# Performance work log

Hardware: AMD Instinct MI355X
Metric: run time of the kernel (lower is better)

The kernel has to match this reference:

```python
import jax, jax.numpy as jnp
import numpy as np

D_MODEL = 1024
NUM_HEADS = 16
DEPTH = D_MODEL // NUM_HEADS


def setup_inputs() -> dict:
    key = jax.random.key(0)
    ks = jax.random.split(key, 9)
    B, S = 2, 2048
    s = 1.0 / np.sqrt(D_MODEL)
    return {
        "x": jax.random.normal(ks[0], (B, S, D_MODEL), dtype=jnp.float32),
        "wq": jax.random.normal(ks[1], (D_MODEL, D_MODEL), dtype=jnp.float32) * s,
        "bq": jnp.zeros((D_MODEL,), dtype=jnp.float32),
        "wk": jax.random.normal(ks[2], (D_MODEL, D_MODEL), dtype=jnp.float32) * s,
        "bk": jnp.zeros((D_MODEL,), dtype=jnp.float32),
        "wv": jax.random.normal(ks[3], (D_MODEL, D_MODEL), dtype=jnp.float32) * s,
        "bv": jnp.zeros((D_MODEL,), dtype=jnp.float32),
        "wo": jax.random.normal(ks[4], (D_MODEL, D_MODEL), dtype=jnp.float32) * s,
        "bo": jnp.zeros((D_MODEL,), dtype=jnp.float32),
    }


def _split_heads(t):
    # [B, S, D] -> [B, H, S, depth]
    B, S, _ = t.shape
    return t.reshape(B, S, NUM_HEADS, DEPTH).transpose(0, 2, 1, 3)


def reference(x, wq, bq, wk, bk, wv, bv, wo, bo):
    B, S, _ = x.shape
    q = _split_heads(x @ wq + bq)
    k = _split_heads(x @ wk + bk)
    v = _split_heads(x @ wv + bv)
    scale = 1.0 / jnp.sqrt(jnp.asarray(DEPTH, dtype=x.dtype))
    logits = jnp.einsum("bhsd,bhtd->bhst", q, k) * scale  # [B,H,S,S]
    attn = jax.nn.softmax(logits, axis=-1)
    ctx = jnp.einsum("bhst,bhtd->bhsd", attn, v)  # [B,H,S,depth]
    concat = ctx.transpose(0, 2, 1, 3).reshape(B, S, D_MODEL)
    return concat @ wo + bo
```

## Files before the change

### kernel.cpp

```cpp
#include <hip/hip_runtime.h>
#include <hip/hip_bf16.h>

typedef __bf16 bf16;
typedef __bf16 bf16x4 __attribute__((ext_vector_type(4)));
typedef __bf16 bf16x8 __attribute__((ext_vector_type(8)));
typedef float f32x4 __attribute__((ext_vector_type(4)));

#define D_MODEL 1024
#define NHEAD 16
#define DEPTH 64
#define SEQ 2048
#define BATCH 2
#define NTOK (BATCH * SEQ)

#define Q_SCALE 0.18033688f

__global__ __launch_bounds__(256) void convert_f32_bf16(const float* __restrict__ src,
                                                        bf16* __restrict__ dst) {
    int i = blockIdx.x * 256 + threadIdx.x;
    float4 v = ((const float4*)src)[i];
    bf16x4 o = {(bf16)v.x, (bf16)v.y, (bf16)v.z, (bf16)v.w};
    *(bf16x4*)&dst[(size_t)i * 4] = o;
}

__global__ __launch_bounds__(256) void transpose_convert(const float* __restrict__ w0,
                                                         const float* __restrict__ w1,
                                                         const float* __restrict__ w2,
                                                         const float* __restrict__ w3,
                                                         bf16* __restrict__ dst) {
    int z = blockIdx.z;
    const float* w = (z == 0) ? w0 : (z == 1) ? w1 : (z == 2) ? w2 : w3;
    bf16* d = dst + (size_t)z * D_MODEL * D_MODEL;
    __shared__ float tile[32][33];
    int c0 = blockIdx.x * 32;
    int r0 = blockIdx.y * 32;
    int tx = threadIdx.x, ty = threadIdx.y;
#pragma unroll
    for (int i = 0; i < 4; i++)
        tile[ty + i * 8][tx] = w[(size_t)(r0 + ty + i * 8) * D_MODEL + c0 + tx];
    __syncthreads();
#pragma unroll
    for (int i = 0; i < 4; i++)
        d[(size_t)(c0 + ty + i * 8) * D_MODEL + r0 + tx] = (bf16)tile[tx][ty + i * 8];
}

__device__ __forceinline__ void gemm_core(const bf16* __restrict__ A,
                                          const bf16* __restrict__ Bt,
                                          int row0, int col0,
                                          bf16* As, bf16* Bs, f32x4 acc[4][4]) {
    const int tid = threadIdx.x;
    const int lane = tid & 63, wave = tid >> 6;
    const int quad = lane >> 4, l16 = lane & 15;
    const int wm = (wave & 1) << 6, wn = (wave >> 1) << 6;
    const int sr = tid >> 1, sh = (tid & 1) << 4;

    for (int k0 = 0; k0 < D_MODEL; k0 += 32) {
        bf16x8 a0 = *(const bf16x8*)&A[(size_t)(row0 + sr) * D_MODEL + k0 + sh];
        bf16x8 a1 = *(const bf16x8*)&A[(size_t)(row0 + sr) * D_MODEL + k0 + sh + 8];
        bf16x8 b0 = *(const bf16x8*)&Bt[(size_t)(col0 + sr) * D_MODEL + k0 + sh];
        bf16x8 b1 = *(const bf16x8*)&Bt[(size_t)(col0 + sr) * D_MODEL + k0 + sh + 8];
        __syncthreads();
        *(bf16x8*)&As[sr * 40 + sh] = a0;
        *(bf16x8*)&As[sr * 40 + sh + 8] = a1;
        *(bf16x8*)&Bs[sr * 40 + sh] = b0;
        *(bf16x8*)&Bs[sr * 40 + sh + 8] = b1;
        __syncthreads();
        bf16x8 af[4], bfr[4];
#pragma unroll
        for (int i = 0; i < 4; i++)
            af[i] = *(const bf16x8*)&As[(wm + i * 16 + l16) * 40 + quad * 8];
#pragma unroll
        for (int j = 0; j < 4; j++)
            bfr[j] = *(const bf16x8*)&Bs[(wn + j * 16 + l16) * 40 + quad * 8];
#pragma unroll
        for (int i = 0; i < 4; i++)
#pragma unroll
            for (int j = 0; j < 4; j++)
                acc[i][j] = __builtin_amdgcn_mfma_f32_16x16x32_bf16(af[i], bfr[j], acc[i][j], 0, 0, 0);
    }
}

__global__ __launch_bounds__(256) void qkv_gemm(const bf16* __restrict__ xb,
                                                const bf16* __restrict__ wtb,
                                                const float* __restrict__ bq,
                                                const float* __restrict__ bk,
                                                const float* __restrict__ bv,
                                                bf16* __restrict__ q,
                                                bf16* __restrict__ k,
                                                bf16* __restrict__ v) {
    __shared__ bf16 As[128 * 40];
    __shared__ bf16 Bs[128 * 40];
    int z = blockIdx.z;
    const bf16* Bt = wtb + (size_t)z * D_MODEL * D_MODEL;
    const float* bias = (z == 0) ? bq : (z == 1) ? bk : bv;
    int row0 = blockIdx.y * 128, col0 = blockIdx.x * 128;
    f32x4 acc[4][4] = {};
    gemm_core(xb, Bt, row0, col0, As, Bs, acc);

    const int lane = threadIdx.x & 63, wave = threadIdx.x >> 6;
    const int quad = lane >> 4, l16 = lane & 15;
    const int wm = (wave & 1) << 6, wn = (wave >> 1) << 6;
    bf16* dst = (z == 0) ? q : (z == 1) ? k : v;
    const float sc = (z == 0) ? Q_SCALE : 1.0f;
#pragma unroll
    for (int i = 0; i < 4; i++) {
#pragma unroll
        for (int j = 0; j < 4; j++) {
            int colg = col0 + wn + j * 16 + l16;
            int hh = colg >> 6, d = colg & 63;
            float bi = bias[colg];
            int rbase = row0 + wm + i * 16 + quad * 4;
            int b = rbase >> 11;
            int sb = rbase & 2047;
            if (z < 2) {
#pragma unroll
                for (int r = 0; r < 4; r++) {
                    size_t idx = ((size_t)(b * NHEAD + hh) * SEQ + sb + r) * DEPTH + d;
                    dst[idx] = (bf16)((acc[i][j][r] + bi) * sc);
                }
            } else {
                bf16x4 pv = {(bf16)(acc[i][j][0] + bi), (bf16)(acc[i][j][1] + bi),
                             (bf16)(acc[i][j][2] + bi), (bf16)(acc[i][j][3] + bi)};
                *(bf16x4*)&dst[((size_t)(b * NHEAD + hh) * DEPTH + d) * SEQ + sb] = pv;
            }
        }
    }
}

__global__ __launch_bounds__(256) void attn(const bf16* __restrict__ q,
                                            const bf16* __restrict__ k,
                                            const bf16* __restrict__ v,
                                            bf16* __restrict__ ctx) {
    __shared__ bf16 Ks[64 * 72];
    __shared__ bf16 Vs[64 * 72];
    __shared__ bf16 Ps[4][32 * 72];
    const int tid = threadIdx.x;
    const int lane = tid & 63, wave = tid >> 6;
    const int quad = lane >> 4, l16 = lane & 15;
    const int bh = blockIdx.y;
    const int q0 = blockIdx.x * 128;
    const size_t hb = (size_t)bh * SEQ * DEPTH;
    const bf16* qh = q + hb;
    const bf16* kh = k + hb;
    const bf16* vh = v + hb;

    bf16x8 bq_[2][2];
#pragma unroll
    for (int g = 0; g < 2; g++) {
        int qrow = q0 + wave * 32 + g * 16 + l16;
#pragma unroll
        for (int c = 0; c < 2; c++)
            bq_[g][c] = *(const bf16x8*)&qh[(size_t)qrow * DEPTH + c * 32 + quad * 8];
    }
    bf16* myP = &Ps[wave][0];

    bf16x8 ones;
#pragma unroll
    for (int i = 0; i < 8; i++) ones[i] = (bf16)1.0f;

    f32x4 ov[2][4] = {};
    f32x4 lacc[2] = {};

    const int srow = tid >> 2, scol = (tid & 3) << 4;
    const bf16* kg = kh + (size_t)srow * DEPTH + scol;
    const bf16* vg = vh + (size_t)srow * SEQ + scol;
    bf16* ksd = &Ks[srow * 72 + scol];
    bf16* vsd = &Vs[srow * 72 + scol];

    bf16x8 kr0 = *(const bf16x8*)kg, kr1 = *(const bf16x8*)(kg + 8);
    bf16x8 vr0 = *(const bf16x8*)vg, vr1 = *(const bf16x8*)(vg + 8);

    for (int t0 = 0; t0 < SEQ; t0 += 64) {
        __syncthreads();
        *(bf16x8*)ksd = kr0;  *(bf16x8*)(ksd + 8) = kr1;
        *(bf16x8*)vsd = vr0;  *(bf16x8*)(vsd + 8) = vr1;
        __syncthreads();
        if (t0 + 64 < SEQ) {
            const bf16* kgn = kg + (size_t)(t0 + 64) * DEPTH;
            const bf16* vgn = vg + (t0 + 64);
            kr0 = *(const bf16x8*)kgn;  kr1 = *(const bf16x8*)(kgn + 8);
            vr0 = *(const bf16x8*)vgn;  vr1 = *(const bf16x8*)(vgn + 8);
        }
        f32x4 sc[2][4] = {};
#pragma unroll
        for (int c = 0; c < 2; c++)
#pragma unroll
            for (int j = 0; j < 4; j++) {
                bf16x8 kf = *(const bf16x8*)&Ks[(j * 16 + l16) * 72 + c * 32 + quad * 8];
#pragma unroll
                for (int g = 0; g < 2; g++)
                    sc[g][j] = __builtin_amdgcn_mfma_f32_16x16x32_bf16(kf, bq_[g][c], sc[g][j], 0, 0, 0);
            }
#pragma unroll
        for (int g = 0; g < 2; g++)
#pragma unroll
            for (int j = 0; j < 4; j++) {
                bf16x4 pb = {(bf16)__builtin_amdgcn_exp2f(sc[g][j][0]),
                             (bf16)__builtin_amdgcn_exp2f(sc[g][j][1]),
                             (bf16)__builtin_amdgcn_exp2f(sc[g][j][2]),
                             (bf16)__builtin_amdgcn_exp2f(sc[g][j][3])};
                *(bf16x4*)&myP[(g * 16 + l16) * 72 + j * 16 + quad * 4] = pb;
            }
#pragma unroll
        for (int c = 0; c < 2; c++) {
            bf16x8 pf[2];
#pragma unroll
            for (int g = 0; g < 2; g++) {
                pf[g] = *(const bf16x8*)&myP[(g * 16 + l16) * 72 + c * 32 + quad * 8];
                lacc[g] = __builtin_amdgcn_mfma_f32_16x16x32_bf16(ones, pf[g], lacc[g], 0, 0, 0);
            }
#pragma unroll
            for (int t = 0; t < 4; t++) {
                bf16x8 vf = *(const bf16x8*)&Vs[(t * 16 + l16) * 72 + c * 32 + quad * 8];
#pragma unroll
                for (int g = 0; g < 2; g++)
                    ov[g][t] = __builtin_amdgcn_mfma_f32_16x16x32_bf16(vf, pf[g], ov[g][t], 0, 0, 0);
            }
        }
    }
    int b = bh >> 4, hh = bh & 15;
#pragma unroll
    for (int g = 0; g < 2; g++) {
        float inv = 1.0f / lacc[g][0];
        size_t rowb = ((size_t)(b * SEQ + q0 + wave * 32 + g * 16 + l16)) * D_MODEL + hh * 64;
#pragma unroll
        for (int t = 0; t < 4; t++) {
            bf16x4 ob = {(bf16)(ov[g][t][0] * inv), (bf16)(ov[g][t][1] * inv),
                         (bf16)(ov[g][t][2] * inv), (bf16)(ov[g][t][3] * inv)};
            *(bf16x4*)&ctx[rowb + t * 16 + quad * 4] = ob;
        }
    }
}

__global__ __launch_bounds__(256) void out_gemm(const bf16* __restrict__ ctx,
                                                const bf16* __restrict__ wot,
                                                const float* __restrict__ bo,
                                                float* __restrict__ out) {
    __shared__ bf16 As[128 * 40];
    __shared__ bf16 Bs[128 * 40];
    int row0 = blockIdx.y * 128, col0 = blockIdx.x * 128;
    f32x4 acc[4][4] = {};
    gemm_core(ctx, wot, row0, col0, As, Bs, acc);

    const int lane = threadIdx.x & 63, wave = threadIdx.x >> 6;
    const int quad = lane >> 4, l16 = lane & 15;
    const int wm = (wave & 1) << 6, wn = (wave >> 1) << 6;
#pragma unroll
    for (int i = 0; i < 4; i++)
#pragma unroll
        for (int j = 0; j < 4; j++) {
            int colg = col0 + wn + j * 16 + l16;
            float bi = bo[colg];
            int rbase = row0 + wm + i * 16 + quad * 4;
#pragma unroll
            for (int r = 0; r < 4; r++)
                out[(size_t)(rbase + r) * D_MODEL + colg] = acc[i][j][r] + bi;
        }
}

extern "C" void kernel_launch(void* const* d_in, const int* in_sizes, int n_in,
                              void* d_out, int out_size, void* d_ws, size_t ws_size,
                              hipStream_t stream) {
    const float* x  = (const float*)d_in[0];
    const float* wq = (const float*)d_in[1];
    const float* bq = (const float*)d_in[2];
    const float* wk = (const float*)d_in[3];
    const float* bk = (const float*)d_in[4];
    const float* wv = (const float*)d_in[5];
    const float* bv = (const float*)d_in[6];
    const float* wo = (const float*)d_in[7];
    const float* bo = (const float*)d_in[8];
    float* out = (float*)d_out;

    const size_t MB = 1024 * 1024;
    char* ws = (char*)d_ws;
    bf16* xb  = (bf16*)(ws);
    bf16* wtb = (bf16*)(ws + 8 * MB);
    bf16* qb  = (bf16*)(ws + 16 * MB);
    bf16* kb  = (bf16*)(ws + 24 * MB);
    bf16* vb  = (bf16*)(ws + 32 * MB);
    bf16* ctx = (bf16*)(ws + 40 * MB);

    convert_f32_bf16<<<NTOK * D_MODEL / 1024, 256, 0, stream>>>(x, xb);
    transpose_convert<<<dim3(32, 32, 4), dim3(32, 8), 0, stream>>>(wq, wk, wv, wo, wtb);
    qkv_gemm<<<dim3(8, 32, 3), 256, 0, stream>>>(xb, wtb, bq, bk, bv, qb, kb, vb);
    attn<<<dim3(SEQ / 128, BATCH * NHEAD), 256, 0, stream>>>(qb, kb, vb, ctx);
    out_gemm<<<dim3(8, 32), 256, 0, stream>>>(ctx, wtb + 3 * (size_t)D_MODEL * D_MODEL, bo, out);
}
```

Measured before the change: 208.8 us.

## Split attention over KV chunks with reduction kernel and use direct global-to-LDS GEMM loads

Attention is split into two KV chunks along a new grid dimension. Each chunk writes unnormalized fp32 partial outputs and row sums, and a new reduce kernel combines them into ctx. This is enabled only when the workspace is large enough. The GEMM core now loads tiles with global_load_lds straight into unpadded LDS, and the V projection uses swapped MFMA operands with a new scatter epilogue. The split raises occupancy but adds partial-buffer traffic and an extra launch, and the unpadded LDS may cause bank conflicts.

```diff
diff --git a/kernel.cpp b/kernel.cpp
--- a/kernel.cpp
+++ b/kernel.cpp
@@ -5,6 +5,9 @@
 typedef __bf16 bf16x4 __attribute__((ext_vector_type(4)));
 typedef __bf16 bf16x8 __attribute__((ext_vector_type(8)));
 typedef float f32x4 __attribute__((ext_vector_type(4)));
+
+typedef __attribute__((address_space(3))) void lds_void;
+typedef const __attribute__((address_space(1))) void gbl_void;
 
 #define D_MODEL 1024
 #define NHEAD 16
@@ -12,6 +15,7 @@
 #define SEQ 2048
 #define BATCH 2
 #define NTOK (BATCH * SEQ)
+#define ROWS (BATCH * NHEAD * SEQ)
 
 #define Q_SCALE 0.18033688f
 
@@ -44,6 +48,7 @@
         d[(size_t)(c0 + ty + i * 8) * D_MODEL + r0 + tx] = (bf16)tile[tx][ty + i * 8];
 }
 
+template <bool SWAP>
 __device__ __forceinline__ void gemm_core(const bf16* __restrict__ A,
                                           const bf16* __restrict__ Bt,
                                           int row0, int col0,
@@ -52,31 +57,33 @@
     const int lane = tid & 63, wave = tid >> 6;
     const int quad = lane >> 4, l16 = lane & 15;
     const int wm = (wave & 1) << 6, wn = (wave >> 1) << 6;
-    const int sr = tid >> 1, sh = (tid & 1) << 4;
+    const int srow = lane >> 2, selem = (lane & 3) * 8;
 
     for (int k0 = 0; k0 < D_MODEL; k0 += 32) {
-        bf16x8 a0 = *(const bf16x8*)&A[(size_t)(row0 + sr) * D_MODEL + k0 + sh];
-        bf16x8 a1 = *(const bf16x8*)&A[(size_t)(row0 + sr) * D_MODEL + k0 + sh + 8];
-        bf16x8 b0 = *(const bf16x8*)&Bt[(size_t)(col0 + sr) * D_MODEL + k0 + sh];
-        bf16x8 b1 = *(const bf16x8*)&Bt[(size_t)(col0 + sr) * D_MODEL + k0 + sh + 8];
         __syncthreads();
-        *(bf16x8*)&As[sr * 40 + sh] = a0;
-        *(bf16x8*)&As[sr * 40 + sh + 8] = a1;
-        *(bf16x8*)&Bs[sr * 40 + sh] = b0;
-        *(bf16x8*)&Bs[sr * 40 + sh + 8] = b1;
+#pragma unroll
+        for (int t = 0; t < 2; t++) {
+            int m = wave * 2 + t;
+            const bf16* ga = A + (size_t)(row0 + m * 16 + srow) * D_MODEL + k0 + selem;
+            const bf16* gb = Bt + (size_t)(col0 + m * 16 + srow) * D_MODEL + k0 + selem;
+            __builtin_amdgcn_global_load_lds((gbl_void*)ga, (lds_void*)(As + m * 512 + lane * 8), 16, 0, 0);
+            __builtin_amdgcn_global_load_lds((gbl_void*)gb, (lds_void*)(Bs + m * 512 + lane * 8), 16, 0, 0);
+        }
         __syncthreads();
         bf16x8 af[4], bfr[4];
 #pragma unroll
         for (int i = 0; i < 4; i++)
-            af[i] = *(const bf16x8*)&As[(wm + i * 16 + l16) * 40 + quad * 8];
+            af[i] = *(const bf16x8*)&As[(wm + i * 16 + l16) * 32 + quad * 8];
 #pragma unroll
         for (int j = 0; j < 4; j++)
-            bfr[j] = *(const bf16x8*)&Bs[(wn + j * 16 + l16) * 40 + quad * 8];
+            bfr[j] = *(const bf16x8*)&Bs[(wn + j * 16 + l16) * 32 + quad * 8];
 #pragma unroll
         for (int i = 0; i < 4; i++)
 #pragma unroll
             for (int j = 0; j < 4; j++)
-                acc[i][j] = __builtin_amdgcn_mfma_f32_16x16x32_bf16(af[i], bfr[j], acc[i][j], 0, 0, 0);
+                acc[i][j] = SWAP
+                    ? __builtin_amdgcn_mfma_f32_16x16x32_bf16(bfr[j], af[i], acc[i][j], 0, 0, 0)
+                    : __builtin_amdgcn_mfma_f32_16x16x32_bf16(af[i], bfr[j], acc[i][j], 0, 0, 0);
     }
 }
 
@@ -88,40 +95,53 @@
                                                 bf16* __restrict__ q,
                                                 bf16* __restrict__ k,
                                                 bf16* __restrict__ v) {
-    __shared__ bf16 As[128 * 40];
-    __shared__ bf16 Bs[128 * 40];
+    __shared__ bf16 As[128 * 32];
+    __shared__ bf16 Bs[128 * 32];
     int z = blockIdx.z;
     const bf16* Bt = wtb + (size_t)z * D_MODEL * D_MODEL;
     const float* bias = (z == 0) ? bq : (z == 1) ? bk : bv;
     int row0 = blockIdx.y * 128, col0 = blockIdx.x * 128;
     f32x4 acc[4][4] = {};
-    gemm_core(xb, Bt, row0, col0, As, Bs, acc);
 
     const int lane = threadIdx.x & 63, wave = threadIdx.x >> 6;
     const int quad = lane >> 4, l16 = lane & 15;
     const int wm = (wave & 1) << 6, wn = (wave >> 1) << 6;
-    bf16* dst = (z == 0) ? q : (z == 1) ? k : v;
-    const float sc = (z == 0) ? Q_SCALE : 1.0f;
-#pragma unroll
-    for (int i = 0; i < 4; i++) {
-#pragma unroll
-        for (int j = 0; j < 4; j++) {
-            int colg = col0 + wn + j * 16 + l16;
-            int hh = colg >> 6, d = colg & 63;
-            float bi = bias[colg];
-            int rbase = row0 + wm + i * 16 + quad * 4;
-            int b = rbase >> 11;
-            int sb = rbase & 2047;
-            if (z < 2) {
+
+    if (z < 2) {
+        gemm_core<false>(xb, Bt, row0, col0, As, Bs, acc);
+        bf16* dst = (z == 0) ? q : k;
+        const float sc = (z == 0) ? Q_SCALE : 1.0f;
+#pragma unroll
+        for (int i = 0; i < 4; i++) {
+#pragma unroll
+            for (int j = 0; j < 4; j++) {
+                int colg = col0 + wn + j * 16 + l16;
+                int hh = colg >> 6, d = colg & 63;
+                float bi = bias[colg];
+                int rbase = row0 + wm + i * 16 + quad * 4;
+                int b = rbase >> 11, sb = rbase & 2047;
 #pragma unroll
                 for (int r = 0; r < 4; r++) {
                     size_t idx = ((size_t)(b * NHEAD + hh) * SEQ + sb + r) * DEPTH + d;
                     dst[idx] = (bf16)((acc[i][j][r] + bi) * sc);
                 }
-            } else {
-                bf16x4 pv = {(bf16)(acc[i][j][0] + bi), (bf16)(acc[i][j][1] + bi),
-                             (bf16)(acc[i][j][2] + bi), (bf16)(acc[i][j][3] + bi)};
-                *(bf16x4*)&dst[((size_t)(b * NHEAD + hh) * DEPTH + d) * SEQ + sb] = pv;
+            }
+        }
+    } else {
+        gemm_core<true>(xb, Bt, row0, col0, As, Bs, acc);
+#pragma unroll
+        for (int i = 0; i < 4; i++) {
+            int tok = row0 + wm + i * 16 + l16;
+            int b = tok >> 11, sb = tok & 2047;
+#pragma unroll
+            for (int j = 0; j < 4; j++) {
+#pragma unroll
+                for (int r = 0; r < 4; r++) {
+                    int f = col0 + wn + j * 16 + quad * 4 + r;
+                    int hh = f >> 6, d = f & 63;
+                    v[((size_t)(b * NHEAD + hh) * DEPTH + d) * SEQ + sb] =
+                        (bf16)(acc[i][j][r] + bias[f]);
+                }
             }
         }
     }
@@ -130,7 +150,10 @@
 __global__ __launch_bounds__(256) void attn(const bf16* __restrict__ q,
                                             const bf16* __restrict__ k,
                                             const bf16* __restrict__ v,
-                                            bf16* __restrict__ ctx) {
+                                            bf16* __restrict__ ctx,
+                                            float* __restrict__ ovp,
+                                            float* __restrict__ lp,
+                                            int kv_chunk) {
     __shared__ bf16 Ks[64 * 72];
     __shared__ bf16 Vs[64 * 72];
     __shared__ bf16 Ps[4][32 * 72];
@@ -139,6 +162,8 @@
     const int quad = lane >> 4, l16 = lane & 15;
     const int bh = blockIdx.y;
     const int q0 = blockIdx.x * 128;
+    const int kv0 = blockIdx.z * kv_chunk;
+    const int kv_end = kv0 + kv_chunk;
     const size_t hb = (size_t)bh * SEQ * DEPTH;
     const bf16* qh = q + hb;
     const bf16* kh = k + hb;
@@ -167,15 +192,17 @@
     bf16* ksd = &Ks[srow * 72 + scol];
     bf16* vsd = &Vs[srow * 72 + scol];
 
-    bf16x8 kr0 = *(const bf16x8*)kg, kr1 = *(const bf16x8*)(kg + 8);
-    bf16x8 vr0 = *(const bf16x8*)vg, vr1 = *(const bf16x8*)(vg + 8);
-
-    for (int t0 = 0; t0 < SEQ; t0 += 64) {
+    bf16x8 kr0 = *(const bf16x8*)(kg + (size_t)kv0 * DEPTH);
+    bf16x8 kr1 = *(const bf16x8*)(kg + (size_t)kv0 * DEPTH + 8);
+    bf16x8 vr0 = *(const bf16x8*)(vg + kv0);
+    bf16x8 vr1 = *(const bf16x8*)(vg + kv0 + 8);
+
+    for (int t0 = kv0; t0 < kv_end; t0 += 64) {
         __syncthreads();
         *(bf16x8*)ksd = kr0;  *(bf16x8*)(ksd + 8) = kr1;
         *(bf16x8*)vsd = vr0;  *(bf16x8*)(vsd + 8) = vr1;
         __syncthreads();
-        if (t0 + 64 < SEQ) {
+        if (t0 + 64 < kv_end) {
             const bf16* kgn = kg + (size_t)(t0 + 64) * DEPTH;
             const bf16* vgn = vg + (t0 + 64);
             kr0 = *(const bf16x8*)kgn;  kr1 = *(const bf16x8*)(kgn + 8);
@@ -218,29 +245,64 @@
             }
         }
     }
+    if (ovp) {
+        size_t zb = (size_t)blockIdx.z * ROWS;
+#pragma unroll
+        for (int g = 0; g < 2; g++) {
+            int s = q0 + wave * 32 + g * 16 + l16;
+            size_t row = zb + (size_t)bh * SEQ + s;
+#pragma unroll
+            for (int t = 0; t < 4; t++)
+                *(f32x4*)&ovp[row * DEPTH + t * 16 + quad * 4] = ov[g][t];
+            if (quad == 0) lp[row] = lacc[g][0];
+        }
+    } else {
+        int b = bh >> 4, hh = bh & 15;
+#pragma unroll
+        for (int g = 0; g < 2; g++) {
+            float inv = 1.0f / lacc[g][0];
+            size_t rowb = ((size_t)(b * SEQ + q0 + wave * 32 + g * 16 + l16)) * D_MODEL + hh * 64;
+#pragma unroll
+            for (int t = 0; t < 4; t++) {
+                bf16x4 ob = {(bf16)(ov[g][t][0] * inv), (bf16)(ov[g][t][1] * inv),
+                             (bf16)(ov[g][t][2] * inv), (bf16)(ov[g][t][3] * inv)};
+                *(bf16x4*)&ctx[rowb + t * 16 + quad * 4] = ob;
+            }
+        }
+    }
+}
+
+__global__ __launch_bounds__(256) void reduce_ctx(const float* __restrict__ ovp,
+                                                  const float* __restrict__ lp,
+                                                  bf16* __restrict__ ctx,
+                                                  int ksplit) {
+    int idx = blockIdx.x * 256 + threadIdx.x;
+    int d4 = idx & 15;
+    size_t row = (size_t)(idx >> 4);
+    f32x4 o = {};
+    float l = 0.f;
+    for (int z = 0; z < ksplit; z++) {
+        o += *(const f32x4*)&ovp[((size_t)z * ROWS + row) * DEPTH + d4 * 4];
+        l += lp[(size_t)z * ROWS + row];
+    }
+    float inv = 1.0f / l;
+    int bh = (int)(row >> 11);
+    int s = (int)(row & 2047);
     int b = bh >> 4, hh = bh & 15;
-#pragma unroll
-    for (int g = 0; g < 2; g++) {
-        float inv = 1.0f / lacc[g][0];
-        size_t rowb = ((size_t)(b * SEQ + q0 + wave * 32 + g * 16 + l16)) * D_MODEL + hh * 64;
-#pragma unroll
-        for (int t = 0; t < 4; t++) {
-            bf16x4 ob = {(bf16)(ov[g][t][0] * inv), (bf16)(ov[g][t][1] * inv),
-                         (bf16)(ov[g][t][2] * inv), (bf16)(ov[g][t][3] * inv)};
-            *(bf16x4*)&ctx[rowb + t * 16 + quad * 4] = ob;
-        }
-    }
+    bf16x4 ob = {(bf16)(o[0] * inv), (bf16)(o[1] * inv),
+                 (bf16)(o[2] * inv), (bf16)(o[3] * inv)};
+    *(bf16x4*)&ctx[((size_t)(b * SEQ + s)) * D_MODEL + hh * 64 + d4 * 4] = ob;
 }
 
 __global__ __launch_bounds__(256) void out_gemm(const bf16* __restrict__ ctx,
                                                 const bf16* __restrict__ wot,
                                                 const float* __restrict__ bo,
                                                 float* __restrict__ out) {
-    __shared__ bf16 As[128 * 40];
-    __shared__ bf16 Bs[128 * 40];
+    __shared__ bf16 As[128 * 32];
+    __shared__ bf16 Bs[128 * 32];
     int row0 = blockIdx.y * 128, col0 = blockIdx.x * 128;
     f32x4 acc[4][4] = {};
-    gemm_core(ctx, wot, row0, col0, As, Bs, acc);
+    gemm_core<false>(ctx, wot, row0, col0, As, Bs, acc);
 
     const int lane = threadIdx.x & 63, wave = threadIdx.x >> 6;
     const int quad = lane >> 4, l16 = lane & 15;
@@ -280,10 +342,21 @@
     bf16* kb  = (bf16*)(ws + 24 * MB);
     bf16* vb  = (bf16*)(ws + 32 * MB);
     bf16* ctx = (bf16*)(ws + 40 * MB);
+    float* ovp = (float*)(ws + 48 * MB);
+    float* lp  = (float*)(ws + 82 * MB);
+
+    const int ksplit = (ws_size >= 84 * MB) ? 2 : 0;
 
     convert_f32_bf16<<<NTOK * D_MODEL / 1024, 256, 0, stream>>>(x, xb);
     transpose_convert<<<dim3(32, 32, 4), dim3(32, 8), 0, stream>>>(wq, wk, wv, wo, wtb);
     qkv_gemm<<<dim3(8, 32, 3), 256, 0, stream>>>(xb, wtb, bq, bk, bv, qb, kb, vb);
-    attn<<<dim3(SEQ / 128, BATCH * NHEAD), 256, 0, stream>>>(qb, kb, vb, ctx);
+    if (ksplit == 2) {
+        attn<<<dim3(SEQ / 128, BATCH * NHEAD, 2), 256, 0, stream>>>(
+            qb, kb, vb, ctx, ovp, lp, SEQ / 2);
+        reduce_ctx<<<ROWS * 16 / 256, 256, 0, stream>>>(ovp, lp, ctx, 2);
+    } else {
+        attn<<<dim3(SEQ / 128, BATCH * NHEAD, 1), 256, 0, stream>>>(
+            qb, kb, vb, ctx, nullptr, nullptr, SEQ);
+    }
     out_gemm<<<dim3(8, 32), 256, 0, stream>>>(ctx, wtb + 3 * (size_t)D_MODEL * D_MODEL, bo, out);
 }
```

Result: slower. 224.0 us (+7.3%).

## Use direct global-to-LDS loads in GEMMs, swap MFMA operands, retile out_gemm

Applied to the files above, without the earlier changes.

Replaces the register-staged global-to-shared copies in the GEMM core with global_load_lds direct transfers into an unpadded LDS layout. In qkv_gemm the MFMA operands are swapped so each lane holds four consecutive features, which lets Q and K be written as bf16x4 vector stores. The V stores become scalar. out_gemm is retiled to 64x128 blocks, doubling the grid to raise occupancy. The unpadded 32-element LDS rows may add bank conflicts on the fragment reads, and the loop still has no double buffering.

```diff
diff --git a/kernel.cpp b/kernel.cpp
--- a/kernel.cpp
+++ b/kernel.cpp
@@ -5,6 +5,9 @@
 typedef __bf16 bf16x4 __attribute__((ext_vector_type(4)));
 typedef __bf16 bf16x8 __attribute__((ext_vector_type(8)));
 typedef float f32x4 __attribute__((ext_vector_type(4)));
+
+typedef __attribute__((address_space(3))) void lds_void;
+typedef const __attribute__((address_space(1))) void gbl_void;
 
 #define D_MODEL 1024
 #define NHEAD 16
@@ -44,6 +47,7 @@
         d[(size_t)(c0 + ty + i * 8) * D_MODEL + r0 + tx] = (bf16)tile[tx][ty + i * 8];
 }
 
+template <bool SWAP>
 __device__ __forceinline__ void gemm_core(const bf16* __restrict__ A,
                                           const bf16* __restrict__ Bt,
                                           int row0, int col0,
@@ -52,31 +56,33 @@
     const int lane = tid & 63, wave = tid >> 6;
     const int quad = lane >> 4, l16 = lane & 15;
     const int wm = (wave & 1) << 6, wn = (wave >> 1) << 6;
-    const int sr = tid >> 1, sh = (tid & 1) << 4;
+    const int srow = lane >> 2, selem = (lane & 3) * 8;
 
     for (int k0 = 0; k0 < D_MODEL; k0 += 32) {
-        bf16x8 a0 = *(const bf16x8*)&A[(size_t)(row0 + sr) * D_MODEL + k0 + sh];
-        bf16x8 a1 = *(const bf16x8*)&A[(size_t)(row0 + sr) * D_MODEL + k0 + sh + 8];
-        bf16x8 b0 = *(const bf16x8*)&Bt[(size_t)(col0 + sr) * D_MODEL + k0 + sh];
-        bf16x8 b1 = *(const bf16x8*)&Bt[(size_t)(col0 + sr) * D_MODEL + k0 + sh + 8];
-        __syncthreads();
-        *(bf16x8*)&As[sr * 40 + sh] = a0;
-        *(bf16x8*)&As[sr * 40 + sh + 8] = a1;
-        *(bf16x8*)&Bs[sr * 40 + sh] = b0;
-        *(bf16x8*)&Bs[sr * 40 + sh + 8] = b1;
+        __syncthreads();
+#pragma unroll
+        for (int t = 0; t < 2; t++) {
+            int m = wave * 2 + t;
+            const bf16* ga = A + (size_t)(row0 + m * 16 + srow) * D_MODEL + k0 + selem;
+            const bf16* gb = Bt + (size_t)(col0 + m * 16 + srow) * D_MODEL + k0 + selem;
+            __builtin_amdgcn_global_load_lds((gbl_void*)ga, (lds_void*)(As + m * 512 + lane * 8), 16, 0, 0);
+            __builtin_amdgcn_global_load_lds((gbl_void*)gb, (lds_void*)(Bs + m * 512 + lane * 8), 16, 0, 0);
+        }
         __syncthreads();
         bf16x8 af[4], bfr[4];
 #pragma unroll
         for (int i = 0; i < 4; i++)
-            af[i] = *(const bf16x8*)&As[(wm + i * 16 + l16) * 40 + quad * 8];
+            af[i] = *(const bf16x8*)&As[(wm + i * 16 + l16) * 32 + quad * 8];
 #pragma unroll
         for (int j = 0; j < 4; j++)
-            bfr[j] = *(const bf16x8*)&Bs[(wn + j * 16 + l16) * 40 + quad * 8];
+            bfr[j] = *(const bf16x8*)&Bs[(wn + j * 16 + l16) * 32 + quad * 8];
 #pragma unroll
         for (int i = 0; i < 4; i++)
 #pragma unroll
             for (int j = 0; j < 4; j++)
-                acc[i][j] = __builtin_amdgcn_mfma_f32_16x16x32_bf16(af[i], bfr[j], acc[i][j], 0, 0, 0);
+                acc[i][j] = SWAP
+                    ? __builtin_amdgcn_mfma_f32_16x16x32_bf16(bfr[j], af[i], acc[i][j], 0, 0, 0)
+                    : __builtin_amdgcn_mfma_f32_16x16x32_bf16(af[i], bfr[j], acc[i][j], 0, 0, 0);
     }
 }
 
@@ -88,40 +94,51 @@
                                                 bf16* __restrict__ q,
                                                 bf16* __restrict__ k,
                                                 bf16* __restrict__ v) {
-    __shared__ bf16 As[128 * 40];
-    __shared__ bf16 Bs[128 * 40];
+    __shared__ bf16 As[128 * 32];
+    __shared__ bf16 Bs[128 * 32];
     int z = blockIdx.z;
     const bf16* Bt = wtb + (size_t)z * D_MODEL * D_MODEL;
     const float* bias = (z == 0) ? bq : (z == 1) ? bk : bv;
     int row0 = blockIdx.y * 128, col0 = blockIdx.x * 128;
     f32x4 acc[4][4] = {};
-    gemm_core(xb, Bt, row0, col0, As, Bs, acc);
+    gemm_core<true>(xb, Bt, row0, col0, As, Bs, acc);
 
     const int lane = threadIdx.x & 63, wave = threadIdx.x >> 6;
     const int quad = lane >> 4, l16 = lane & 15;
     const int wm = (wave & 1) << 6, wn = (wave >> 1) << 6;
-    bf16* dst = (z == 0) ? q : (z == 1) ? k : v;
-    const float sc = (z == 0) ? Q_SCALE : 1.0f;
-#pragma unroll
-    for (int i = 0; i < 4; i++) {
-#pragma unroll
-        for (int j = 0; j < 4; j++) {
-            int colg = col0 + wn + j * 16 + l16;
-            int hh = colg >> 6, d = colg & 63;
-            float bi = bias[colg];
-            int rbase = row0 + wm + i * 16 + quad * 4;
-            int b = rbase >> 11;
-            int sb = rbase & 2047;
-            if (z < 2) {
+    if (z < 2) {
+        bf16* dst = (z == 0) ? q : k;
+        const float sc = (z == 0) ? Q_SCALE : 1.0f;
+#pragma unroll
+        for (int i = 0; i < 4; i++) {
+            int tok = row0 + wm + i * 16 + l16;
+            int b = tok >> 11, sb = tok & 2047;
+#pragma unroll
+            for (int j = 0; j < 4; j++) {
+                int f0 = col0 + wn + j * 16 + quad * 4;
+                int hh = f0 >> 6, d0 = f0 & 63;
+                f32x4 bi = *(const f32x4*)&bias[f0];
+                bf16x4 ob = {(bf16)((acc[i][j][0] + bi[0]) * sc),
+                             (bf16)((acc[i][j][1] + bi[1]) * sc),
+                             (bf16)((acc[i][j][2] + bi[2]) * sc),
+                             (bf16)((acc[i][j][3] + bi[3]) * sc)};
+                *(bf16x4*)&dst[((size_t)(b * NHEAD + hh) * SEQ + sb) * DEPTH + d0] = ob;
+            }
+        }
+    } else {
+#pragma unroll
+        for (int i = 0; i < 4; i++) {
+            int tok = row0 + wm + i * 16 + l16;
+            int b = tok >> 11, sb = tok & 2047;
+#pragma unroll
+            for (int j = 0; j < 4; j++) {
 #pragma unroll
                 for (int r = 0; r < 4; r++) {
-                    size_t idx = ((size_t)(b * NHEAD + hh) * SEQ + sb + r) * DEPTH + d;
-                    dst[idx] = (bf16)((acc[i][j][r] + bi) * sc);
+                    int f = col0 + wn + j * 16 + quad * 4 + r;
+                    int hh = f >> 6, d = f & 63;
+                    v[((size_t)(b * NHEAD + hh) * DEPTH + d) * SEQ + sb] =
+                        (bf16)(acc[i][j][r] + bias[f]);
                 }
-            } else {
-                bf16x4 pv = {(bf16)(acc[i][j][0] + bi), (bf16)(acc[i][j][1] + bi),
-                             (bf16)(acc[i][j][2] + bi), (bf16)(acc[i][j][3] + bi)};
-                *(bf16x4*)&dst[((size_t)(b * NHEAD + hh) * DEPTH + d) * SEQ + sb] = pv;
             }
         }
     }
@@ -236,22 +253,48 @@
                                                 const bf16* __restrict__ wot,
                                                 const float* __restrict__ bo,
                                                 float* __restrict__ out) {
-    __shared__ bf16 As[128 * 40];
-    __shared__ bf16 Bs[128 * 40];
-    int row0 = blockIdx.y * 128, col0 = blockIdx.x * 128;
-    f32x4 acc[4][4] = {};
-    gemm_core(ctx, wot, row0, col0, As, Bs, acc);
-
-    const int lane = threadIdx.x & 63, wave = threadIdx.x >> 6;
+    __shared__ bf16 As[64 * 32];
+    __shared__ bf16 Bs[128 * 32];
+    const int tid = threadIdx.x;
+    const int lane = tid & 63, wave = tid >> 6;
     const int quad = lane >> 4, l16 = lane & 15;
-    const int wm = (wave & 1) << 6, wn = (wave >> 1) << 6;
+    const int srow = lane >> 2, selem = (lane & 3) * 8;
+    int row0 = blockIdx.y * 64, col0 = blockIdx.x * 128;
+    f32x4 acc[4][2] = {};
+
+    for (int k0 = 0; k0 < D_MODEL; k0 += 32) {
+        __syncthreads();
+        {
+            const bf16* ga = ctx + (size_t)(row0 + wave * 16 + srow) * D_MODEL + k0 + selem;
+            __builtin_amdgcn_global_load_lds((gbl_void*)ga, (lds_void*)(As + wave * 512 + lane * 8), 16, 0, 0);
+        }
+#pragma unroll
+        for (int t = 0; t < 2; t++) {
+            int m = wave * 2 + t;
+            const bf16* gb = wot + (size_t)(col0 + m * 16 + srow) * D_MODEL + k0 + selem;
+            __builtin_amdgcn_global_load_lds((gbl_void*)gb, (lds_void*)(Bs + m * 512 + lane * 8), 16, 0, 0);
+        }
+        __syncthreads();
+        bf16x8 af[4], bfr[2];
+#pragma unroll
+        for (int i = 0; i < 4; i++)
+            af[i] = *(const bf16x8*)&As[(i * 16 + l16) * 32 + quad * 8];
+#pragma unroll
+        for (int j = 0; j < 2; j++)
+            bfr[j] = *(const bf16x8*)&Bs[(wave * 32 + j * 16 + l16) * 32 + quad * 8];
+#pragma unroll
+        for (int i = 0; i < 4; i++)
+#pragma unroll
+            for (int j = 0; j < 2; j++)
+                acc[i][j] = __builtin_amdgcn_mfma_f32_16x16x32_bf16(af[i], bfr[j], acc[i][j], 0, 0, 0);
+    }
 #pragma unroll
     for (int i = 0; i < 4; i++)
 #pragma unroll
-        for (int j = 0; j < 4; j++) {
-            int colg = col0 + wn + j * 16 + l16;
+        for (int j = 0; j < 2; j++) {
+            int colg = col0 + wave * 32 + j * 16 + l16;
             float bi = bo[colg];
-            int rbase = row0 + wm + i * 16 + quad * 4;
+            int rbase = row0 + i * 16 + quad * 4;
 #pragma unroll
             for (int r = 0; r < 4; r++)
                 out[(size_t)(rbase + r) * D_MODEL + colg] = acc[i][j][r] + bi;
@@ -285,5 +328,5 @@
     transpose_convert<<<dim3(32, 32, 4), dim3(32, 8), 0, stream>>>(wq, wk, wv, wo, wtb);
     qkv_gemm<<<dim3(8, 32, 3), 256, 0, stream>>>(xb, wtb, bq, bk, bv, qb, kb, vb);
     attn<<<dim3(SEQ / 128, BATCH * NHEAD), 256, 0, stream>>>(qb, kb, vb, ctx);
-    out_gemm<<<dim3(8, 32), 256, 0, stream>>>(ctx, wtb + 3 * (size_t)D_MODEL * D_MODEL, bo, out);
-}
+    out_gemm<<<dim3(8, 64), 256, 0, stream>>>(ctx, wtb + 3 * (size_t)D_MODEL * D_MODEL, bo, out);
+}
```

Result: slower. 225.0 us (+7.7%).
